# Kernel tuning notes

Hardware: AMD Instinct MI355X
Metric: run time of the kernel (lower is better)

The kernel has to match this reference:

```python
import jax, jax.numpy as jnp
import numpy as np

B, N = 2048, 4096

def setup_inputs() -> dict:
    key = jax.random.key(0)
    k1, k2, k3 = jax.random.split(key, 3)
    keypoints = jax.random.normal(k1, (B, 3, N), dtype=jnp.float32)
    pseudo = jax.random.normal(k2, (B, 3, N), dtype=jnp.float32)
    weight = jax.random.uniform(k3, (B, 1, N), dtype=jnp.float32)
    return {"keypoints": keypoints, "pseudo": pseudo, "weight": weight}


def reference(keypoints, pseudo, weight):
    # keypoints, pseudo: [B,3,N]; weight: [B,1,N]
    w = jnp.sum(weight, axis=2, keepdims=True)                      # [B,1,1]
    wT = jnp.swapaxes(weight, 1, 2)                                 # [B,N,1]
    kp_centroid = (keypoints @ wT) / w                              # [B,3,1]
    ps_centroid = (pseudo @ wT) / w                                 # [B,3,1]
    kp_centered = keypoints - kp_centroid                           # [B,3,N]
    ps_centered = pseudo - ps_centroid                              # [B,3,N]
    # weighted cross-covariance H = (1/w) * (kp_c * weight) @ ps_c^T  -> [B,3,3]
    H = ((kp_centered * weight) @ jnp.swapaxes(ps_centered, 1, 2)) / w
    U, S, Vh = jnp.linalg.svd(H)                                    # H = U S Vh
    V = jnp.swapaxes(Vh, 1, 2)                                      # [B,3,3]
    Ut = jnp.swapaxes(U, 1, 2)
    R0 = V @ Ut
    det = jnp.linalg.det(R0)                                        # [B]
    d = jnp.where(det < 0, -1.0, 1.0).astype(H.dtype)               # [B]
    # flip last column of V where det < 0 (branch-free reflection fix)
    scale = jnp.stack([jnp.ones_like(d), jnp.ones_like(d), d], axis=-1)[:, None, :]  # [B,1,3]
    R = (V * scale) @ Ut                                            # [B,3,3]
    t = -(R @ (kp_centroid - jnp.swapaxes(R, 1, 2) @ ps_centroid))  # [B,3,1]
    t = t[..., 0]                                                   # [B,3]
    return (R, t)
```

## Files before the change

### kernel.cpp

```cpp
#include <hip/hip_runtime.h>
#include <math.h>

constexpr int Bn = 2048;
constexpr int Nn = 4096;
constexpr int TPB = 256;

struct G {
    float4 w4, k0, k1, k2, p0, p1, p2;
};

__device__ __forceinline__ G loadg(const float* __restrict__ wb,
                                   const float* __restrict__ kpb,
                                   const float* __restrict__ psb,
                                   int idx)
{
    G g;
    g.w4 = *reinterpret_cast<const float4*>(wb + idx);
    g.k0 = *reinterpret_cast<const float4*>(kpb + idx);
    g.k1 = *reinterpret_cast<const float4*>(kpb + Nn + idx);
    g.k2 = *reinterpret_cast<const float4*>(kpb + 2 * Nn + idx);
    g.p0 = *reinterpret_cast<const float4*>(psb + idx);
    g.p1 = *reinterpret_cast<const float4*>(psb + Nn + idx);
    g.p2 = *reinterpret_cast<const float4*>(psb + 2 * Nn + idx);
    return g;
}

__global__ __launch_bounds__(TPB, 4)
void kabsch_all(const float* __restrict__ kp,
                const float* __restrict__ ps,
                const float* __restrict__ wt,
                float* __restrict__ out)
{
    const int b   = blockIdx.x;
    const int tid = threadIdx.x;
    const float* kpb = kp + (size_t)b * 3 * Nn;
    const float* psb = ps + (size_t)b * 3 * Nn;
    const float* wb  = wt + (size_t)b * Nn;

    const int i0 = tid * 4;
    const int i1 = i0 + 1024;
    const int i2 = i0 + 2048;
    const int i3 = i0 + 3072;

    float acc[16];
#pragma unroll
    for (int i = 0; i < 16; ++i) acc[i] = 0.f;

#define ACCUM(GG, C) do {                                               \
        const float wj = GG.w4.C;                                       \
        const float a0 = GG.k0.C, a1 = GG.k1.C, a2 = GG.k2.C;           \
        const float q0 = GG.p0.C, q1 = GG.p1.C, q2 = GG.p2.C;           \
        const float wa0 = wj * a0, wa1 = wj * a1, wa2 = wj * a2;        \
        acc[0]  += wj;                                                  \
        acc[1]  += wa0;      acc[2]  += wa1;      acc[3]  += wa2;       \
        acc[4]  += wj * q0;  acc[5]  += wj * q1;  acc[6]  += wj * q2;   \
        acc[7]  += wa0 * q0; acc[8]  += wa0 * q1; acc[9]  += wa0 * q2;  \
        acc[10] += wa1 * q0; acc[11] += wa1 * q1; acc[12] += wa1 * q2;  \
        acc[13] += wa2 * q0; acc[14] += wa2 * q1; acc[15] += wa2 * q2;  \
    } while (0)
#define CONSUME(GG) ACCUM(GG, x); ACCUM(GG, y); ACCUM(GG, z); ACCUM(GG, w)

    G g0 = loadg(wb, kpb, psb, i0);
    G g1 = loadg(wb, kpb, psb, i1);
    CONSUME(g0);
    G g2 = loadg(wb, kpb, psb, i2);
    CONSUME(g1);
    G g3 = loadg(wb, kpb, psb, i3);
    CONSUME(g2);
    CONSUME(g3);
#undef CONSUME
#undef ACCUM

#pragma unroll
    for (int i = 0; i < 16; ++i) {
        float v = acc[i];
#pragma unroll
        for (int off = 32; off > 0; off >>= 1) v += __shfl_down(v, off);
        acc[i] = v;
    }

    __shared__ float red[4][16];
    const int lane = tid & 63;
    const int wid  = tid >> 6;
    if (lane == 0) {
#pragma unroll
        for (int i = 0; i < 16; ++i) red[wid][i] = acc[i];
    }
    __syncthreads();
    if (tid != 0) return;

    double s[16];
#pragma unroll
    for (int i = 0; i < 16; ++i)
        s[i] = (double)red[0][i] + (double)red[1][i] +
               (double)red[2][i] + (double)red[3][i];

    const double W    = s[0];
    const double invW = 1.0 / W;
    double kc[3] = { s[1] * invW, s[2] * invW, s[3] * invW };
    double pc[3] = { s[4] * invW, s[5] * invW, s[6] * invW };
    double H[3][3];
#pragma unroll
    for (int i = 0; i < 3; ++i)
#pragma unroll
        for (int j = 0; j < 3; ++j)
            H[i][j] = s[7 + i * 3 + j] * invW - kc[i] * pc[j];

    double A[3][3];
#pragma unroll
    for (int i = 0; i < 3; ++i)
#pragma unroll
        for (int j = 0; j < 3; ++j)
            A[i][j] = H[0][i] * H[0][j] + H[1][i] * H[1][j] + H[2][i] * H[2][j];

    double V[3][3] = { {1,0,0}, {0,1,0}, {0,0,1} };

#define JROT(P,Q) do {                                                       \
        const double apq = A[P][Q];                                          \
        if (fabs(apq) > 1e-300) {                                            \
            const double th = (A[Q][Q] - A[P][P]) / (2.0 * apq);             \
            const double tt = copysign(1.0, th) / (fabs(th) + sqrt(1.0 + th * th)); \
            const double cc = 1.0 / sqrt(1.0 + tt * tt);                     \
            const double sn = tt * cc;                                       \
            _Pragma("unroll")                                                \
            for (int k = 0; k < 3; ++k) {                                    \
                const double akp = A[k][P], akq = A[k][Q];                   \
                A[k][P] = cc * akp - sn * akq;                               \
                A[k][Q] = sn * akp + cc * akq;                               \
            }                                                                \
            _Pragma("unroll")                                                \
            for (int k = 0; k < 3; ++k) {                                    \
                const double apk = A[P][k], aqk = A[Q][k];                   \
                A[P][k] = cc * apk - sn * aqk;                               \
                A[Q][k] = sn * apk + cc * aqk;                               \
            }                                                                \
            _Pragma("unroll")                                                \
            for (int k = 0; k < 3; ++k) {                                    \
                const double vkp = V[k][P], vkq = V[k][Q];                   \
                V[k][P] = cc * vkp - sn * vkq;                               \
                V[k][Q] = sn * vkp + cc * vkq;                               \
            }                                                                \
        }                                                                    \
    } while (0)

    for (int sweep = 0; sweep < 6; ++sweep) { JROT(0,1); JROT(0,2); JROT(1,2); }
#undef JROT

    double lam[3] = { A[0][0], A[1][1], A[2][2] };
#define CSWAP(I,J) if (lam[I] < lam[J]) {                                    \
        const double tl = lam[I]; lam[I] = lam[J]; lam[J] = tl;              \
        _Pragma("unroll")                                                    \
        for (int k = 0; k < 3; ++k) {                                        \
            const double tv = V[k][I]; V[k][I] = V[k][J]; V[k][J] = tv; }    \
    }
    CSWAP(0, 1); CSWAP(0, 2); CSWAP(1, 2);
#undef CSWAP

    double v0[3] = { V[0][0], V[1][0], V[2][0] };
    double v1[3] = { V[0][1], V[1][1], V[2][1] };
    double v2[3] = { v0[1] * v1[2] - v0[2] * v1[1],
                     v0[2] * v1[0] - v0[0] * v1[2],
                     v0[0] * v1[1] - v0[1] * v1[0] };

    double u0[3], u1[3];
#pragma unroll
    for (int i = 0; i < 3; ++i)
        u0[i] = H[i][0] * v0[0] + H[i][1] * v0[1] + H[i][2] * v0[2];
    {
        double n0 = sqrt(u0[0]*u0[0] + u0[1]*u0[1] + u0[2]*u0[2]);
        n0 = fmax(n0, 1e-300);
#pragma unroll
        for (int i = 0; i < 3; ++i) u0[i] /= n0;
    }
    {
        double b1[3];
#pragma unroll
        for (int i = 0; i < 3; ++i)
            b1[i] = H[i][0] * v1[0] + H[i][1] * v1[1] + H[i][2] * v1[2];
        const double dp = u0[0]*b1[0] + u0[1]*b1[1] + u0[2]*b1[2];
#pragma unroll
        for (int i = 0; i < 3; ++i) b1[i] -= dp * u0[i];
        double n1 = sqrt(b1[0]*b1[0] + b1[1]*b1[1] + b1[2]*b1[2]);
        if (n1 > 1e-150) {
#pragma unroll
            for (int i = 0; i < 3; ++i) u1[i] = b1[i] / n1;
        } else {
            double e[3] = { 0, 0, 0 };
            if (fabs(u0[0]) <= fabs(u0[1]) && fabs(u0[0]) <= fabs(u0[2])) e[0] = 1;
            else if (fabs(u0[1]) <= fabs(u0[2])) e[1] = 1;
            else e[2] = 1;
            double c1[3] = { u0[1]*e[2] - u0[2]*e[1],
                             u0[2]*e[0] - u0[0]*e[2],
                             u0[0]*e[1] - u0[1]*e[0] };
            double nc = sqrt(c1[0]*c1[0] + c1[1]*c1[1] + c1[2]*c1[2]);
            nc = fmax(nc, 1e-300);
#pragma unroll
            for (int i = 0; i < 3; ++i) u1[i] = c1[i] / nc;
        }
    }

    const double detH =
        H[0][0] * (H[1][1] * H[2][2] - H[1][2] * H[2][1]) -
        H[0][1] * (H[1][0] * H[2][2] - H[1][2] * H[2][0]) +
        H[0][2] * (H[1][0] * H[2][1] - H[1][1] * H[2][0]);
    const double d = (detH < 0.0) ? -1.0 : 1.0;

    double u2[3] = { d * (u0[1]*u1[2] - u0[2]*u1[1]),
                     d * (u0[2]*u1[0] - u0[0]*u1[2]),
                     d * (u0[0]*u1[1] - u0[1]*u1[0]) };

    double R[3][3];
#pragma unroll
    for (int i = 0; i < 3; ++i)
#pragma unroll
        for (int j = 0; j < 3; ++j)
            R[i][j] = v0[i] * u0[j] + v1[i] * u1[j] + d * v2[i] * u2[j];

    double t[3];
#pragma unroll
    for (int i = 0; i < 3; ++i)
        t[i] = pc[i] - (R[i][0] * kc[0] + R[i][1] * kc[1] + R[i][2] * kc[2]);

    float* outR = out + (size_t)b * 9;
    float* outT = out + (size_t)Bn * 9 + (size_t)b * 3;
#pragma unroll
    for (int i = 0; i < 3; ++i)
#pragma unroll
        for (int j = 0; j < 3; ++j)
            outR[i * 3 + j] = (float)R[i][j];
#pragma unroll
    for (int i = 0; i < 3; ++i) outT[i] = (float)t[i];
}

extern "C" void kernel_launch(void* const* d_in, const int* in_sizes, int n_in,
                              void* d_out, int out_size, void* d_ws, size_t ws_size,
                              hipStream_t stream) {
    const float* kp = (const float*)d_in[0];
    const float* ps = (const float*)d_in[1];
    const float* wt = (const float*)d_in[2];
    float* out = (float*)d_out;
    kabsch_all<<<Bn, TPB, 0, stream>>>(kp, ps, wt, out);
}
```

Measured before the change: 52.51 us.

## Split streaming reduction and per-batch SVD epilogue into separate kernels

The fused kernel is split in two. The streaming kernel now only reduces the 16 weighted moments per batch and writes them to workspace. A second kernel then runs the double-precision 3x3 SVD and rotation solve with one thread per batch. This takes the long serial single-thread tail off the bandwidth-bound blocks and raises the occupancy hint to 8, at the cost of an extra launch and a small workspace round trip. The epilogue now sums the per-wave partials in float rather than double, which slightly changes precision.

```diff
diff --git a/kernel.cpp b/kernel.cpp
--- a/kernel.cpp
+++ b/kernel.cpp
@@ -25,11 +25,11 @@
     return g;
 }
 
-__global__ __launch_bounds__(TPB, 4)
-void kabsch_all(const float* __restrict__ kp,
-                const float* __restrict__ ps,
-                const float* __restrict__ wt,
-                float* __restrict__ out)
+__global__ __launch_bounds__(TPB, 8)
+void kabsch_stream(const float* __restrict__ kp,
+                   const float* __restrict__ ps,
+                   const float* __restrict__ wt,
+                   float* __restrict__ ws)
 {
     const int b   = blockIdx.x;
     const int tid = threadIdx.x;
@@ -38,9 +38,6 @@
     const float* wb  = wt + (size_t)b * Nn;
 
     const int i0 = tid * 4;
-    const int i1 = i0 + 1024;
-    const int i2 = i0 + 2048;
-    const int i3 = i0 + 3072;
 
     float acc[16];
 #pragma unroll
@@ -61,11 +58,11 @@
 #define CONSUME(GG) ACCUM(GG, x); ACCUM(GG, y); ACCUM(GG, z); ACCUM(GG, w)
 
     G g0 = loadg(wb, kpb, psb, i0);
-    G g1 = loadg(wb, kpb, psb, i1);
+    G g1 = loadg(wb, kpb, psb, i0 + 1024);
     CONSUME(g0);
-    G g2 = loadg(wb, kpb, psb, i2);
+    G g2 = loadg(wb, kpb, psb, i0 + 2048);
     CONSUME(g1);
-    G g3 = loadg(wb, kpb, psb, i3);
+    G g3 = loadg(wb, kpb, psb, i0 + 3072);
     CONSUME(g2);
     CONSUME(g3);
 #undef CONSUME
@@ -87,13 +84,22 @@
         for (int i = 0; i < 16; ++i) red[wid][i] = acc[i];
     }
     __syncthreads();
-    if (tid != 0) return;
-
+    if (tid < 16) {
+        const float v = red[0][tid] + red[1][tid] + red[2][tid] + red[3][tid];
+        ws[(size_t)b * 16 + tid] = v;
+    }
+}
+
+__global__ void kabsch_epilogue(const float* __restrict__ ws,
+                                float* __restrict__ out)
+{
+    const int b = blockIdx.x * blockDim.x + threadIdx.x;
+    if (b >= Bn) return;
+
+    const float* p = ws + (size_t)b * 16;
     double s[16];
 #pragma unroll
-    for (int i = 0; i < 16; ++i)
-        s[i] = (double)red[0][i] + (double)red[1][i] +
-               (double)red[2][i] + (double)red[3][i];
+    for (int i = 0; i < 16; ++i) s[i] = (double)p[i];
 
     const double W    = s[0];
     const double invW = 1.0 / W;
@@ -239,5 +245,7 @@
     const float* ps = (const float*)d_in[1];
     const float* wt = (const float*)d_in[2];
     float* out = (float*)d_out;
-    kabsch_all<<<Bn, TPB, 0, stream>>>(kp, ps, wt, out);
-}
+    float* ws  = (float*)d_ws;
+    kabsch_stream<<<Bn, TPB, 0, stream>>>(kp, ps, wt, ws);
+    kabsch_epilogue<<<(Bn + 255) / 256, 256, 0, stream>>>(ws, out);
+}
```

New measurement: 81.96 us. +56.1%, slower.
